# Performance work log

Measured on AMD Instinct MI355X. Metric: run time of the kernel, lower is better.

Reference implementation:

```python
import jax, jax.numpy as jnp
import numpy as np

N = 12288
E = 393216
D_IN, D_HID, D_OUT = 128, 128, 64


def gcn_conv(x, edge_index, W, b, num_nodes):
    # PyG GCNConv: h = x @ W; add self-loops; sym-normalize; scatter-add; + b
    h = x @ W  # [N, F]
    row, col = edge_index[0], edge_index[1]
    sl = jnp.arange(num_nodes, dtype=edge_index.dtype)
    row = jnp.concatenate([row, sl])
    col = jnp.concatenate([col, sl])
    deg = jax.ops.segment_sum(jnp.ones_like(col, dtype=h.dtype), col, num_segments=num_nodes)
    dinv = jax.lax.rsqrt(jnp.maximum(deg, 1e-12))
    norm = dinv[row] * dinv[col]  # [E+N]
    msgs = h[row] * norm[:, None]
    out = jax.ops.segment_sum(msgs, col, num_segments=num_nodes)
    return out + b


def setup_inputs() -> dict:
    key = jax.random.key(0)
    k1, k2, k3, k4, k5 = jax.random.split(key, 5)
    x = jax.random.uniform(k1, (N, D_IN), dtype=jnp.float32)
    edge_index = jax.random.randint(k2, (2, E), 0, N, dtype=jnp.int64)
    # Glorot-style init for GCN weights, zeros for biases (PyG defaults)
    W1 = jax.random.normal(k3, (D_IN, D_HID), dtype=jnp.float32) * (1.0 / np.sqrt(D_IN))
    b1 = jnp.zeros((D_HID,), dtype=jnp.float32)
    W2 = jax.random.normal(k4, (D_HID, D_OUT), dtype=jnp.float32) * (1.0 / np.sqrt(D_HID))
    b2 = jnp.zeros((D_OUT,), dtype=jnp.float32)
    return {"x": x, "edge_index": edge_index, "W1": W1, "b1": b1, "W2": W2, "b2": b2}


def reference(x, edge_index, W1, b1, W2, b2):
    h = jax.nn.relu(gcn_conv(x, edge_index, W1, b1, N))
    latent = gcn_conv(h, edge_index, W2, b2, N)  # [N, D_OUT]
    return latent @ latent.T  # [N, N] gram-matrix decoder
```

## Files before the change

### kernel.cpp

```cpp
#include <hip/hip_runtime.h>

#define NN   12288
#define EE   393216
#define DIN  128
#define DHID 128
#define DOUT 64
#define CAP  96

typedef __attribute__((ext_vector_type(8))) short bf16x8;
typedef __attribute__((ext_vector_type(4))) float f32x4;
typedef __attribute__((ext_vector_type(4))) short s16x4;

__device__ __forceinline__ short f2bf(float f) {
    unsigned u = __float_as_uint(f);
    unsigned r = (u + 0x7fffu + ((u >> 16) & 1u)) >> 16;
    return (short)r;
}
__device__ __forceinline__ float bf2f(short h) {
    return __uint_as_float(((unsigned)(unsigned short)h) << 16);
}

#define GEMM1_BLOCKS 768
#define FILL_BLOCKS  512
__global__ __launch_bounds__(256) void k_fill_gemm1(const float* __restrict__ x,
                                                    const int* __restrict__ row,
                                                    const int* __restrict__ col,
                                                    const float* __restrict__ W1,
                                                    unsigned* __restrict__ cursor,
                                                    int* __restrict__ bucket,
                                                    float* __restrict__ g1) {
    const int b = blockIdx.x, t = threadIdx.x;
    if (b < GEMM1_BLOCKS) {
        __shared__ float xs[16 * DIN];
        const int r0 = b * 16;
        for (int j = t; j < 16 * DIN; j += 256) xs[j] = x[(size_t)r0 * DIN + j];
        __syncthreads();
        const int c = t & 127, rg = (t >> 7) * 8;
        float acc[8] = {};
        for (int k = 0; k < DIN; ++k) {
            float w = W1[k * DHID + c];
#pragma unroll
            for (int r = 0; r < 8; ++r) acc[r] += xs[(rg + r) * DIN + k] * w;
        }
#pragma unroll
        for (int r = 0; r < 8; ++r) g1[(size_t)(r0 + rg + r) * DHID + c] = acc[r];
    } else {
        const int gid = (b - GEMM1_BLOCKS) * 256 + t;
#pragma unroll
        for (int q = 0; q < 3; ++q) {
            int e = gid + q * (FILL_BLOCKS * 256);
            int c = col[e];
            unsigned p = atomicAdd(&cursor[c], 1u);
            if (p < CAP) bucket[(size_t)c * CAP + p] = row[e];
        }
    }
}

__global__ __launch_bounds__(256) void k_gather1_gemm2(const float* __restrict__ g1,
                                                       const int* __restrict__ bucket,
                                                       const unsigned* __restrict__ cursor,
                                                       const float* __restrict__ b1,
                                                       const float* __restrict__ W2,
                                                       float* __restrict__ g2) {
    __shared__ float hs[4][DHID];
    const int lane = threadIdx.x & 63, wave = threadIdx.x >> 6;
    const int c = blockIdx.x * 4 + wave;
    const unsigned cnt = cursor[c];
    const float dc = rsqrtf((float)cnt + 1.0f);
    const unsigned e = cnt < CAP ? cnt : CAP;
    const f32x4* __restrict__ G4 = (const f32x4*)g1;
    const int* __restrict__ bk = bucket + (size_t)c * CAP;
    const int sub = lane >> 5, col4 = lane & 31;

    f32x4 acc = (f32x4){0.f, 0.f, 0.f, 0.f};
    if (sub == 0) acc = G4[(size_t)c * 32 + col4] * dc;

    unsigned i = 0;
    int pr[4];
    if (i + 8 <= e) {
#pragma unroll
        for (int p = 0; p < 4; ++p) pr[p] = bk[i + 2 * p + sub];
    }
    for (; i + 8 <= e;) {
        int r[4];
#pragma unroll
        for (int p = 0; p < 4; ++p) r[p] = pr[p];
        const unsigned ni = i + 8;
        if (ni + 8 <= e) {
#pragma unroll
            for (int p = 0; p < 4; ++p) pr[p] = bk[ni + 2 * p + sub];
        }
        float d[4];
        f32x4 v[4];
#pragma unroll
        for (int p = 0; p < 4; ++p) {
            d[p] = rsqrtf((float)cursor[r[p]] + 1.0f);
            v[p] = G4[(size_t)r[p] * 32 + col4];
        }
#pragma unroll
        for (int p = 0; p < 4; ++p) acc += v[p] * d[p];
        i = ni;
    }
    for (; i + 2 <= e; i += 2) {
        int rr = bk[i + sub];
        float d = rsqrtf((float)cursor[rr] + 1.0f);
        acc += G4[(size_t)rr * 32 + col4] * d;
    }
    if (i < e && sub == 0) {
        int rr = bk[i];
        float d = rsqrtf((float)cursor[rr] + 1.0f);
        acc += G4[(size_t)rr * 32 + col4] * d;
    }
    acc.x += __shfl_xor(acc.x, 32);
    acc.y += __shfl_xor(acc.y, 32);
    acc.z += __shfl_xor(acc.z, 32);
    acc.w += __shfl_xor(acc.w, 32);

    f32x4 bb = ((const f32x4*)b1)[col4];
    f32x4 o = acc * dc + bb;
    o.x = fmaxf(o.x, 0.f);
    o.y = fmaxf(o.y, 0.f);
    o.z = fmaxf(o.z, 0.f);
    o.w = fmaxf(o.w, 0.f);
    if (sub == 0) ((f32x4*)hs[wave])[col4] = o;

    float a2 = 0.f;
#pragma unroll 8
    for (int k = 0; k < DHID; ++k) a2 += hs[wave][k] * W2[k * DOUT + lane];
    g2[(size_t)c * DOUT + lane] = a2 * dc;
}

__global__ __launch_bounds__(256) void k_gather2(const float* __restrict__ g2,
                                                 const int* __restrict__ bucket,
                                                 const unsigned* __restrict__ cursor,
                                                 const float* __restrict__ b2,
                                                 short* __restrict__ H,
                                                 short* __restrict__ Lo) {
    const int lane = threadIdx.x & 63, wave = threadIdx.x >> 6;
    const int c = blockIdx.x * 4 + wave;
    const unsigned cnt = cursor[c];
    const float dc = rsqrtf((float)cnt + 1.0f);
    const unsigned e = cnt < CAP ? cnt : CAP;
    const f32x4* __restrict__ G4 = (const f32x4*)g2;
    const int* __restrict__ bk = bucket + (size_t)c * CAP;
    const int sub = lane >> 4, col4 = lane & 15;

    f32x4 acc = (f32x4){0.f, 0.f, 0.f, 0.f};
    if (sub == 0) acc = G4[(size_t)c * 16 + col4];

    unsigned i = 0;
    int pr0 = 0, pr1 = 0;
    if (i + 8 <= e) { pr0 = bk[i + sub]; pr1 = bk[i + 4 + sub]; }
    for (; i + 8 <= e;) {
        int r0 = pr0, r1 = pr1;
        const unsigned ni = i + 8;
        if (ni + 8 <= e) { pr0 = bk[ni + sub]; pr1 = bk[ni + 4 + sub]; }
        f32x4 v0 = G4[(size_t)r0 * 16 + col4];
        f32x4 v1 = G4[(size_t)r1 * 16 + col4];
        acc += v0;
        acc += v1;
        i = ni;
    }
    for (; i + 4 <= e; i += 4) {
        int rr = bk[i + sub];
        acc += G4[(size_t)rr * 16 + col4];
    }
    if (i < e) {
        if (sub < (int)(e - i)) {
            int rr = bk[i + sub];
            acc += G4[(size_t)rr * 16 + col4];
        }
    }
    acc.x += __shfl_xor(acc.x, 16); acc.x += __shfl_xor(acc.x, 32);
    acc.y += __shfl_xor(acc.y, 16); acc.y += __shfl_xor(acc.y, 32);
    acc.z += __shfl_xor(acc.z, 16); acc.z += __shfl_xor(acc.z, 32);
    acc.w += __shfl_xor(acc.w, 16); acc.w += __shfl_xor(acc.w, 32);

    if (sub == 0) {
        f32x4 bb = ((const f32x4*)b2)[col4];
        f32x4 v = acc * dc + bb;
        s16x4 h4, l4;
        h4.x = f2bf(v.x); l4.x = f2bf(v.x - bf2f(h4.x));
        h4.y = f2bf(v.y); l4.y = f2bf(v.y - bf2f(h4.y));
        h4.z = f2bf(v.z); l4.z = f2bf(v.z - bf2f(h4.z));
        h4.w = f2bf(v.w); l4.w = f2bf(v.w - bf2f(h4.w));
        ((s16x4*)H)[(size_t)c * 16 + col4] = h4;
        ((s16x4*)Lo)[(size_t)c * 16 + col4] = l4;
    }
}

#define NTILE 96
#define NPAIR ((NTILE * (NTILE + 1)) / 2)
__global__ __launch_bounds__(256) void k_gram(const short* __restrict__ H,
                                              const short* __restrict__ L,
                                              float* __restrict__ out) {
    __shared__ float P[64][132];
    const int tid  = threadIdx.x;
    const int lane = tid & 63;
    const int wave = tid >> 6;

    const int Lb = blockIdx.x;
    int bi = (int)((193.0f - sqrtf(193.0f * 193.0f - 8.0f * (float)Lb)) * 0.5f);
    if (bi < 0) bi = 0;
    if (bi > NTILE - 1) bi = NTILE - 1;
    while (bi * NTILE - (bi * (bi - 1)) / 2 > Lb) --bi;
    while ((bi + 1) * NTILE - ((bi + 1) * bi) / 2 <= Lb) ++bi;
    const int bj = bi + (Lb - (bi * NTILE - (bi * (bi - 1)) / 2));

    const int wm = wave >> 1, wn = wave & 1;
    const int row0 = bi * 128 + wm * 64;
    const int col0 = bj * 128 + wn * 64;
    const int fr = lane & 15;
    const int fk = (lane >> 4) << 3;
    const int crow = (lane >> 4) * 4;
    const bool mirror = (bi != bj);

    bf16x8 aH[4][2], aL[4][2];
#pragma unroll
    for (int m = 0; m < 4; ++m)
#pragma unroll
        for (int k = 0; k < 2; ++k) {
            size_t off = (size_t)(row0 + m * 16 + fr) * DOUT + k * 32 + fk;
            aH[m][k] = *(const bf16x8*)(H + off);
            aL[m][k] = *(const bf16x8*)(L + off);
        }

    f32x4 acc[4][4];
#pragma unroll
    for (int n = 0; n < 4; ++n)
#pragma unroll
        for (int m = 0; m < 4; ++m) acc[n][m] = (f32x4){0.f, 0.f, 0.f, 0.f};

#pragma unroll
    for (int n = 0; n < 4; ++n) {
        bf16x8 bH[2], bL[2];
#pragma unroll
        for (int k = 0; k < 2; ++k) {
            size_t off = (size_t)(col0 + n * 16 + fr) * DOUT + k * 32 + fk;
            bH[k] = *(const bf16x8*)(H + off);
            bL[k] = *(const bf16x8*)(L + off);
        }
#pragma unroll
        for (int m = 0; m < 4; ++m)
#pragma unroll
            for (int k = 0; k < 2; ++k) {
                acc[n][m] = __builtin_amdgcn_mfma_f32_16x16x32_bf16(aL[m][k], bH[k], acc[n][m], 0, 0, 0);
                acc[n][m] = __builtin_amdgcn_mfma_f32_16x16x32_bf16(aH[m][k], bL[k], acc[n][m], 0, 0, 0);
                acc[n][m] = __builtin_amdgcn_mfma_f32_16x16x32_bf16(aH[m][k], bH[k], acc[n][m], 0, 0, 0);
            }
    }

    const size_t gr0 = (size_t)bi * 128, gc0 = (size_t)bj * 128;
#pragma unroll
    for (int h = 0; h < 2; ++h) {
        __syncthreads();
        if (wm == h) {
#pragma unroll
            for (int n = 0; n < 4; ++n)
#pragma unroll
                for (int m = 0; m < 4; ++m)
#pragma unroll
                    for (int j = 0; j < 4; ++j)
                        P[m * 16 + crow + j][wn * 64 + n * 16 + fr] = acc[n][m][j];
        }
        __syncthreads();
#pragma unroll
        for (int it = 0; it < 8; ++it) {
            int idx = it * 256 + tid;
            int r = idx >> 5, c4 = (idx & 31) << 2;
            f32x4 v = *(const f32x4*)&P[r][c4];
            __builtin_nontemporal_store(v, (f32x4*)&out[(gr0 + h * 64 + r) * NN + gc0 + c4]);
        }
        if (mirror) {
#pragma unroll
            for (int it = 0; it < 8; ++it) {
                int idx = it * 256 + tid;
                int r = idx >> 4, c4 = (idx & 15) << 2;
                f32x4 v;
                v.x = P[c4 + 0][r];
                v.y = P[c4 + 1][r];
                v.z = P[c4 + 2][r];
                v.w = P[c4 + 3][r];
                __builtin_nontemporal_store(v, (f32x4*)&out[(gc0 + r) * NN + gr0 + h * 64 + c4]);
            }
        }
    }
}

extern "C" void kernel_launch(void* const* d_in, const int* in_sizes, int n_in,
                              void* d_out, int out_size, void* d_ws, size_t ws_size,
                              hipStream_t stream) {
    const float* x  = (const float*)d_in[0];
    const int*   ei = (const int*)d_in[1];
    const float* W1 = (const float*)d_in[2];
    const float* b1 = (const float*)d_in[3];
    const float* W2 = (const float*)d_in[4];
    const float* b2 = (const float*)d_in[5];
    float* out = (float*)d_out;

    const int* row = ei;
    const int* col = ei + EE;

    char* w = (char*)d_ws;
    unsigned* cursor = (unsigned*)w; w += (size_t)NN * 4;
    int*      bucket = (int*)w;      w += (size_t)NN * CAP * 4;
    float*    g1     = (float*)w;    w += (size_t)NN * DHID * 4;
    float*    g2     = (float*)w;    w += (size_t)NN * DOUT * 4;
    short*    latH   = (short*)w;    w += (size_t)NN * DOUT * 2;
    short*    latL   = (short*)w;    w += (size_t)NN * DOUT * 2;

    hipMemsetAsync(cursor, 0, (size_t)NN * 4, stream);

    k_fill_gemm1<<<GEMM1_BLOCKS + FILL_BLOCKS, 256, 0, stream>>>(x, row, col, W1, cursor, bucket, g1);
    k_gather1_gemm2<<<NN / 4, 256, 0, stream>>>(g1, bucket, cursor, b1, W2, g2);
    k_gather2<<<NN / 4, 256, 0, stream>>>(g2, bucket, cursor, b2, latH, latL);

    k_gram<<<NPAIR, 256, 0, stream>>>(latH, latL, out);
}
```

Measured before the change: 207.9 us.

## Store first-layer features in bf16 and swizzle gram output staging buffer

The first-layer projection output g1 is now stored as bf16 instead of fp32, which halves the bytes read by the random-access neighbour gather in the first aggregation kernel. Values are converted back to fp32 before accumulation. Separately, the gram kernel's shared-memory staging tile uses an XOR column swizzle to reduce bank conflicts on the transposed mirror reads. The bf16 storage lowers the precision of the intermediate features, which could push results past the tolerance.

```diff
diff --git a/kernel.cpp b/kernel.cpp
--- a/kernel.cpp
+++ b/kernel.cpp
@@ -18,6 +18,11 @@
 }
 __device__ __forceinline__ float bf2f(short h) {
     return __uint_as_float(((unsigned)(unsigned short)h) << 16);
+}
+__device__ __forceinline__ f32x4 cvt4(s16x4 v) {
+    f32x4 o;
+    o.x = bf2f(v.x); o.y = bf2f(v.y); o.z = bf2f(v.z); o.w = bf2f(v.w);
+    return o;
 }
 
 #define GEMM1_BLOCKS 768
@@ -28,7 +33,7 @@
                                                     const float* __restrict__ W1,
                                                     unsigned* __restrict__ cursor,
                                                     int* __restrict__ bucket,
-                                                    float* __restrict__ g1) {
+                                                    short* __restrict__ g1b) {
     const int b = blockIdx.x, t = threadIdx.x;
     if (b < GEMM1_BLOCKS) {
         __shared__ float xs[16 * DIN];
@@ -43,7 +48,7 @@
             for (int r = 0; r < 8; ++r) acc[r] += xs[(rg + r) * DIN + k] * w;
         }
 #pragma unroll
-        for (int r = 0; r < 8; ++r) g1[(size_t)(r0 + rg + r) * DHID + c] = acc[r];
+        for (int r = 0; r < 8; ++r) g1b[(size_t)(r0 + rg + r) * DHID + c] = f2bf(acc[r]);
     } else {
         const int gid = (b - GEMM1_BLOCKS) * 256 + t;
 #pragma unroll
@@ -56,7 +61,7 @@
     }
 }
 
-__global__ __launch_bounds__(256) void k_gather1_gemm2(const float* __restrict__ g1,
+__global__ __launch_bounds__(256) void k_gather1_gemm2(const short* __restrict__ g1b,
                                                        const int* __restrict__ bucket,
                                                        const unsigned* __restrict__ cursor,
                                                        const float* __restrict__ b1,
@@ -68,12 +73,12 @@
     const unsigned cnt = cursor[c];
     const float dc = rsqrtf((float)cnt + 1.0f);
     const unsigned e = cnt < CAP ? cnt : CAP;
-    const f32x4* __restrict__ G4 = (const f32x4*)g1;
+    const s16x4* __restrict__ G4 = (const s16x4*)g1b;
     const int* __restrict__ bk = bucket + (size_t)c * CAP;
     const int sub = lane >> 5, col4 = lane & 31;
 
     f32x4 acc = (f32x4){0.f, 0.f, 0.f, 0.f};
-    if (sub == 0) acc = G4[(size_t)c * 32 + col4] * dc;
+    if (sub == 0) acc = cvt4(G4[(size_t)c * 32 + col4]) * dc;
 
     unsigned i = 0;
     int pr[4];
@@ -91,25 +96,25 @@
             for (int p = 0; p < 4; ++p) pr[p] = bk[ni + 2 * p + sub];
         }
         float d[4];
-        f32x4 v[4];
+        s16x4 v[4];
 #pragma unroll
         for (int p = 0; p < 4; ++p) {
             d[p] = rsqrtf((float)cursor[r[p]] + 1.0f);
             v[p] = G4[(size_t)r[p] * 32 + col4];
         }
 #pragma unroll
-        for (int p = 0; p < 4; ++p) acc += v[p] * d[p];
+        for (int p = 0; p < 4; ++p) acc += cvt4(v[p]) * d[p];
         i = ni;
     }
     for (; i + 2 <= e; i += 2) {
         int rr = bk[i + sub];
         float d = rsqrtf((float)cursor[rr] + 1.0f);
-        acc += G4[(size_t)rr * 32 + col4] * d;
+        acc += cvt4(G4[(size_t)rr * 32 + col4]) * d;
     }
     if (i < e && sub == 0) {
         int rr = bk[i];
         float d = rsqrtf((float)cursor[rr] + 1.0f);
-        acc += G4[(size_t)rr * 32 + col4] * d;
+        acc += cvt4(G4[(size_t)rr * 32 + col4]) * d;
     }
     acc.x += __shfl_xor(acc.x, 32);
     acc.y += __shfl_xor(acc.y, 32);
@@ -260,15 +265,18 @@
 #pragma unroll
                 for (int m = 0; m < 4; ++m)
 #pragma unroll
-                    for (int j = 0; j < 4; ++j)
-                        P[m * 16 + crow + j][wn * 64 + n * 16 + fr] = acc[n][m][j];
+                    for (int j = 0; j < 4; ++j) {
+                        int rw = m * 16 + crow + j;
+                        int cl = (wn * 64 + n * 16 + fr) ^ ((rw & 7) << 2);
+                        P[rw][cl] = acc[n][m][j];
+                    }
         }
         __syncthreads();
 #pragma unroll
         for (int it = 0; it < 8; ++it) {
             int idx = it * 256 + tid;
             int r = idx >> 5, c4 = (idx & 31) << 2;
-            f32x4 v = *(const f32x4*)&P[r][c4];
+            f32x4 v = *(const f32x4*)&P[r][c4 ^ ((r & 7) << 2)];
             __builtin_nontemporal_store(v, (f32x4*)&out[(gr0 + h * 64 + r) * NN + gc0 + c4]);
         }
         if (mirror) {
@@ -277,10 +285,10 @@
                 int idx = it * 256 + tid;
                 int r = idx >> 4, c4 = (idx & 15) << 2;
                 f32x4 v;
-                v.x = P[c4 + 0][r];
-                v.y = P[c4 + 1][r];
-                v.z = P[c4 + 2][r];
-                v.w = P[c4 + 3][r];
+                v.x = P[c4 + 0][r ^ (((c4 + 0) & 7) << 2)];
+                v.y = P[c4 + 1][r ^ (((c4 + 1) & 7) << 2)];
+                v.z = P[c4 + 2][r ^ (((c4 + 2) & 7) << 2)];
+                v.w = P[c4 + 3][r ^ (((c4 + 3) & 7) << 2)];
                 __builtin_nontemporal_store(v, (f32x4*)&out[(gc0 + r) * NN + gr0 + h * 64 + c4]);
             }
         }
@@ -304,15 +312,15 @@
     char* w = (char*)d_ws;
     unsigned* cursor = (unsigned*)w; w += (size_t)NN * 4;
     int*      bucket = (int*)w;      w += (size_t)NN * CAP * 4;
-    float*    g1     = (float*)w;    w += (size_t)NN * DHID * 4;
+    short*    g1b    = (short*)w;    w += (size_t)NN * DHID * 2;
     float*    g2     = (float*)w;    w += (size_t)NN * DOUT * 4;
     short*    latH   = (short*)w;    w += (size_t)NN * DOUT * 2;
     short*    latL   = (short*)w;    w += (size_t)NN * DOUT * 2;
 
     hipMemsetAsync(cursor, 0, (size_t)NN * 4, stream);
 
-    k_fill_gemm1<<<GEMM1_BLOCKS + FILL_BLOCKS, 256, 0, stream>>>(x, row, col, W1, cursor, bucket, g1);
-    k_gather1_gemm2<<<NN / 4, 256, 0, stream>>>(g1, bucket, cursor, b1, W2, g2);
+    k_fill_gemm1<<<GEMM1_BLOCKS + FILL_BLOCKS, 256, 0, stream>>>(x, row, col, W1, cursor, bucket, g1b);
+    k_gather1_gemm2<<<NN / 4, 256, 0, stream>>>(g1b, bucket, cursor, b1, W2, g2);
     k_gather2<<<NN / 4, 256, 0, stream>>>(g2, bucket, cursor, b2, latH, latL);
 
     k_gram<<<NPAIR, 256, 0, stream>>>(latH, latL, out);
```

After: 210.8 us. Within noise of the previous version (+1.4%).
